# Kernel optimization log

Measured on AMD Instinct MI355X. Metric: run time of the kernel, lower is better.

The kernel has to match this reference:

```python
import jax, jax.numpy as jnp
import numpy as np

B, N, D, E, H, F, L = 4096, 32, 128, 256, 8, 1024, 6
DH = E // H  # head dim = 32
LN_EPS = 1e-5


def setup_inputs() -> dict:
    key = jax.random.key(0)
    ks = jax.random.split(key, 8)
    def s(k, shape, fan_in):
        return (jax.random.normal(k, shape, jnp.float32) / np.float32(np.sqrt(fan_in)))
    inp = {
        "obs": jax.random.normal(ks[0], (B, D), jnp.float32),
        "emb_W": s(ks[1], (N, D, E), D),          # per-node tokenizer Linear weights
        "emb_b": jnp.zeros((N, E), jnp.float32),
        "pos_emb": jax.random.normal(ks[2], (N, E), jnp.float32) * 0.02,
        "Wqkv": s(ks[3], (3 * E, E), E),          # shared across all L layers (torch code shares one layer object)
        "bqkv": jnp.zeros((3 * E,), jnp.float32),
        "Wo": s(ks[4], (E, E), E),
        "bo": jnp.zeros((E,), jnp.float32),
        "ln1_g": jnp.ones((E,), jnp.float32),
        "ln1_b": jnp.zeros((E,), jnp.float32),
        "ln2_g": jnp.ones((E,), jnp.float32),
        "ln2_b": jnp.zeros((E,), jnp.float32),
        "W1": s(ks[5], (E, F), E),
        "b1": jnp.zeros((F,), jnp.float32),
        "W2": s(ks[6], (F, E), F),
        "b2": jnp.zeros((E,), jnp.float32),
    }
    # kinematic-chain adjacency (|i-j|<=1) incl. forced self-loops, additive mask
    idx = jnp.arange(N)
    adj = jnp.abs(idx[:, None] - idx[None, :]) <= 1
    inp["adj_mask"] = jnp.where(adj, 0.0, -1e9).astype(jnp.float32)  # [N, N]
    return inp


def _layer_norm(x, g, b):
    m = jnp.mean(x, axis=-1, keepdims=True)
    v = jnp.var(x, axis=-1, keepdims=True)
    return (x - m) * jax.lax.rsqrt(v + LN_EPS) * g + b


def _encoder_layer(x, adj_mask, Wqkv, bqkv, Wo, bo, ln1_g, ln1_b, ln2_g, ln2_b, W1, b1, W2, b2):
    # pre-LN self-attention block
    h = _layer_norm(x, ln1_g, ln1_b)                      # [B, N, E]
    qkv = h @ Wqkv.T + bqkv                               # [B, N, 3E]
    q, k, v = jnp.split(qkv, 3, axis=-1)
    q = q.reshape(B, N, H, DH).transpose(0, 2, 1, 3)      # [B, H, N, DH]
    k = k.reshape(B, N, H, DH).transpose(0, 2, 1, 3)
    v = v.reshape(B, N, H, DH).transpose(0, 2, 1, 3)
    scale = np.float32(1.0 / np.sqrt(DH))
    scores = jnp.einsum('bhqd,bhkd->bhqk', q, k) * scale + adj_mask  # [B, H, N, N]
    attn = jax.nn.softmax(scores, axis=-1)
    o = jnp.einsum('bhqk,bhkd->bhqd', attn, v)
    o = o.transpose(0, 2, 1, 3).reshape(B, N, E)
    x = x + (o @ Wo.T + bo)
    # pre-LN feed-forward block (ReLU)
    h2 = _layer_norm(x, ln2_g, ln2_b)
    x = x + (jax.nn.relu(h2 @ W1 + b1) @ W2 + b2)
    return x


def reference(obs, emb_W, emb_b, pos_emb, Wqkv, bqkv, Wo, bo,
              ln1_g, ln1_b, ln2_g, ln2_b, W1, b1, W2, b2, adj_mask):
    # per-node MLP tokenizer (every node sees full obs): [B,D] x [N,D,E] -> [B,N,E]
    x = jnp.einsum('bd,nde->bne', obs, emb_W) + emb_b + pos_emb
    # BoT-Hard: all L layers masked; torch ModuleList shares a single layer's params
    for _ in range(L):
        x = _encoder_layer(x, adj_mask, Wqkv, bqkv, Wo, bo,
                           ln1_g, ln1_b, ln2_g, ln2_b, W1, b1, W2, b2)
    return x
```

## Files before the change

kernel.cpp:

```cpp
#include <hip/hip_runtime.h>
#include <hip/hip_bf16.h>
#include <stdint.h>

#define B_ 4096
#define N_ 32
#define D_ 128
#define E_ 256
#define H_ 8
#define F_ 1024
#define L_ 6
#define M_ (B_ * N_)

typedef unsigned short u16;
typedef __attribute__((ext_vector_type(8))) short short8;
typedef __attribute__((ext_vector_type(4))) short short4v;
typedef __attribute__((ext_vector_type(4))) float floatx4;

__device__ __forceinline__ float b2f(u16 u) {
  union { unsigned int i; float f; } c;
  c.i = ((unsigned int)u) << 16;
  return c.f;
}
__device__ __forceinline__ u16 f2b(float f) {
  union { float f; unsigned int i; } c;
  c.f = f;
  unsigned int x = c.i;
  return (u16)((x + 0x7fffu + ((x >> 16) & 1u)) >> 16);
}

template <bool RELU, bool RESID, bool OUTF32>
__global__ __launch_bounds__(256) void gemm_bt(
    const u16* __restrict__ A, int lda, long sAz,
    const u16* __restrict__ Bt, long sBz,
    const float* __restrict__ bias, long sBiasz,
    void* __restrict__ Cv, int ldc, long sCz,
    const float* __restrict__ resid,
    int K) {
  __shared__ u16 As[128 * 32];
  __shared__ u16 Bs[128 * 32];
  const int tid = threadIdx.x;
  const int wave = tid >> 6;
  const int lane = tid & 63;
  const int wm = wave & 1;
  const int wn = wave >> 1;
  const int lrow = lane & 15;
  const int quad = lane >> 4;
  const int z = blockIdx.z;
  const long m0 = (long)blockIdx.x * 128;
  const long n0 = (long)blockIdx.y * 128;

  const u16* Ab = A + (long)z * sAz + m0 * lda;
  const u16* Bb = Bt + (long)z * sBz + n0 * K;

  floatx4 acc[4][4];
#pragma unroll
  for (int a = 0; a < 4; ++a)
#pragma unroll
    for (int b = 0; b < 4; ++b) acc[a][b] = floatx4{0.f, 0.f, 0.f, 0.f};

  const int c0 = tid, c1 = tid + 256;
  const int r0 = c0 >> 2, o0 = (c0 & 3) * 8;
  const int r1 = c1 >> 2, o1 = (c1 & 3) * 8;

  for (int kb = 0; kb < K; kb += 32) {
    __syncthreads();
    short8 a0 = *(const short8*)(Ab + (long)r0 * lda + kb + o0);
    short8 a1 = *(const short8*)(Ab + (long)r1 * lda + kb + o1);
    short8 b0 = *(const short8*)(Bb + (long)r0 * K + kb + o0);
    short8 b1 = *(const short8*)(Bb + (long)r1 * K + kb + o1);
    *(short8*)(As + c0 * 8) = a0;
    *(short8*)(As + c1 * 8) = a1;
    *(short8*)(Bs + c0 * 8) = b0;
    *(short8*)(Bs + c1 * 8) = b1;
    __syncthreads();
    short8 af[4], bfr[4];
#pragma unroll
    for (int t = 0; t < 4; ++t) {
      af[t] = *(const short8*)(As + (wm * 64 + t * 16 + lrow) * 32 + quad * 8);
      bfr[t] = *(const short8*)(Bs + (wn * 64 + t * 16 + lrow) * 32 + quad * 8);
    }
#pragma unroll
    for (int tm = 0; tm < 4; ++tm)
#pragma unroll
      for (int tn = 0; tn < 4; ++tn)
        acc[tm][tn] = __builtin_amdgcn_mfma_f32_16x16x32_bf16(af[tm], bfr[tn], acc[tm][tn], 0, 0, 0);
  }

  const long cz = (long)z * sCz;
#pragma unroll
  for (int tn = 0; tn < 4; ++tn) {
    const long col = n0 + wn * 64 + tn * 16 + lrow;
    const float bv = bias[(long)z * sBiasz + col];
#pragma unroll
    for (int tm = 0; tm < 4; ++tm) {
#pragma unroll
      for (int r = 0; r < 4; ++r) {
        const long row = m0 + wm * 64 + tm * 16 + quad * 4 + r;
        float v = acc[tm][tn][r] + bv;
        if (RELU) v = fmaxf(v, 0.0f);
        const long idx = cz + row * (long)ldc + col;
        if (RESID) v += resid[idx];
        if (OUTF32)
          ((float*)Cv)[idx] = v;
        else
          ((u16*)Cv)[idx] = f2b(v);
      }
    }
  }
}

__global__ __launch_bounds__(256) void ln_kernel(const float* __restrict__ x,
                                                 const float* __restrict__ g,
                                                 const float* __restrict__ be,
                                                 u16* __restrict__ out) {
  const long row = ((long)blockIdx.x << 2) | (threadIdx.x >> 6);
  const int lane = threadIdx.x & 63;
  const float* xr = x + row * 256 + lane * 4;
  floatx4 v = *(const floatx4*)xr;
  float s = v[0] + v[1] + v[2] + v[3];
#pragma unroll
  for (int mk = 32; mk >= 1; mk >>= 1) s += __shfl_xor(s, mk, 64);
  const float mean = s * (1.0f / 256.0f);
  floatx4 d;
#pragma unroll
  for (int k = 0; k < 4; ++k) d[k] = v[k] - mean;
  float qs = d[0] * d[0] + d[1] * d[1] + d[2] * d[2] + d[3] * d[3];
#pragma unroll
  for (int mk = 32; mk >= 1; mk >>= 1) qs += __shfl_xor(qs, mk, 64);
  const float rstd = rsqrtf(qs * (1.0f / 256.0f) + 1e-5f);
  const int cb = lane * 4;
  const floatx4 gv = *(const floatx4*)(g + cb);
  const floatx4 bv = *(const floatx4*)(be + cb);
  short4v ov;
#pragma unroll
  for (int k = 0; k < 4; ++k)
    ov[k] = (short)f2b(d[k] * rstd * gv[k] + bv[k]);
  *(short4v*)(out + row * 256 + cb) = ov;
}

__global__ __launch_bounds__(256) void attn_kernel(const u16* __restrict__ qkv,
                                                   u16* __restrict__ o) {
  const int t = blockIdx.x * 256 + threadIdx.x;
  const int i = t & 31;
  const int h = (t >> 5) & 7;
  const long b = (long)(t >> 8);
  const long m = b * 32 + i;
  const u16* qp = qkv + m * 768 + h * 32;
  float q[32];
#pragma unroll
  for (int c = 0; c < 4; ++c) {
    short8 qv = *(const short8*)(qp + c * 8);
#pragma unroll
    for (int k = 0; k < 8; ++k) q[c * 8 + k] = b2f((u16)qv[k]);
  }
  float sc[3];
  int jc[3];
#pragma unroll
  for (int jj = 0; jj < 3; ++jj) {
    const int j = i - 1 + jj;
    const bool valid = (j >= 0) && (j < 32);
    const int jcl = valid ? j : i;
    jc[jj] = jcl;
    const u16* kp = qkv + (b * 32 + jcl) * 768 + 256 + h * 32;
    float dot = 0.0f;
#pragma unroll
    for (int c = 0; c < 4; ++c) {
      short8 kv = *(const short8*)(kp + c * 8);
#pragma unroll
      for (int k = 0; k < 8; ++k) dot += q[c * 8 + k] * b2f((u16)kv[k]);
    }
    sc[jj] = valid ? dot * 0.17677669529663687f : -3.0e38f;
  }
  const float mx = fmaxf(sc[0], fmaxf(sc[1], sc[2]));
  const float w0 = __expf(sc[0] - mx);
  const float w1 = __expf(sc[1] - mx);
  const float w2 = __expf(sc[2] - mx);
  const float inv = 1.0f / (w0 + w1 + w2);
  const float w[3] = {w0 * inv, w1 * inv, w2 * inv};
  float acc[32];
#pragma unroll
  for (int k = 0; k < 32; ++k) acc[k] = 0.0f;
#pragma unroll
  for (int jj = 0; jj < 3; ++jj) {
    const u16* vp = qkv + (b * 32 + jc[jj]) * 768 + 512 + h * 32;
    const float wj = w[jj];
#pragma unroll
    for (int c = 0; c < 4; ++c) {
      short8 vv = *(const short8*)(vp + c * 8);
#pragma unroll
      for (int k = 0; k < 8; ++k) acc[c * 8 + k] += wj * b2f((u16)vv[k]);
    }
  }
  u16* op = o + m * 256 + h * 32;
#pragma unroll
  for (int c = 0; c < 4; ++c) {
    short8 ov;
#pragma unroll
    for (int k = 0; k < 8; ++k) ov[k] = (short)f2b(acc[c * 8 + k]);
    *(short8*)(op + c * 8) = ov;
  }
}

__global__ __launch_bounds__(256) void transpose_f2b(const float* __restrict__ src,
                                                     u16* __restrict__ dst,
                                                     int R, int C) {
  const long base = (long)blockIdx.z * R * C;
  const int idx = blockIdx.x * 256 + threadIdx.x;
  if (idx < R * C) {
    const int r = idx / C;
    const int c = idx - r * C;
    dst[base + (long)c * R + r] = f2b(src[base + idx]);
  }
}

__global__ __launch_bounds__(256) void cvt_f2b_kernel(const float* __restrict__ s,
                                                      u16* __restrict__ d, int n) {
  const int i = blockIdx.x * 256 + threadIdx.x;
  if (i < n) d[i] = f2b(s[i]);
}

__global__ __launch_bounds__(256) void addf_kernel(const float* __restrict__ a,
                                                   const float* __restrict__ b,
                                                   float* __restrict__ d, int n) {
  const int i = blockIdx.x * 256 + threadIdx.x;
  if (i < n) d[i] = a[i] + b[i];
}

extern "C" void kernel_launch(void* const* d_in, const int* in_sizes, int n_in,
                              void* d_out, int out_size, void* d_ws, size_t ws_size,
                              hipStream_t stream) {
  (void)in_sizes; (void)n_in; (void)out_size; (void)ws_size;
  const float* obs   = (const float*)d_in[0];
  const float* emb_W = (const float*)d_in[1];
  const float* emb_b = (const float*)d_in[2];
  const float* pos   = (const float*)d_in[3];
  const float* Wqkv  = (const float*)d_in[4];
  const float* bqkv  = (const float*)d_in[5];
  const float* Wo    = (const float*)d_in[6];
  const float* bo    = (const float*)d_in[7];
  const float* ln1_g = (const float*)d_in[8];
  const float* ln1_b = (const float*)d_in[9];
  const float* ln2_g = (const float*)d_in[10];
  const float* ln2_b = (const float*)d_in[11];
  const float* W1    = (const float*)d_in[12];
  const float* b1    = (const float*)d_in[13];
  const float* W2    = (const float*)d_in[14];
  const float* b2    = (const float*)d_in[15];

  float* x = (float*)d_out;

  char* ws = (char*)d_ws;
  u16* hbuf   = (u16*)ws;   ws += (size_t)M_ * E_ * 2;
  u16* sbuf   = (u16*)ws;   ws += (size_t)M_ * F_ * 2;
  u16* embWt  = (u16*)ws;   ws += (size_t)N_ * D_ * E_ * 2;
  u16* obs_bf = (u16*)ws;   ws += (size_t)B_ * D_ * 2;
  u16* wqkv_bf= (u16*)ws;   ws += (size_t)3 * E_ * E_ * 2;
  u16* wo_bf  = (u16*)ws;   ws += (size_t)E_ * E_ * 2;
  u16* w1t    = (u16*)ws;   ws += (size_t)E_ * F_ * 2;
  u16* w2t    = (u16*)ws;   ws += (size_t)E_ * F_ * 2;
  float* cbias= (float*)ws; ws += (size_t)N_ * E_ * 4;

  transpose_f2b<<<dim3((D_ * E_ + 255) / 256, 1, N_), 256, 0, stream>>>(emb_W, embWt, D_, E_);
  transpose_f2b<<<dim3((E_ * F_ + 255) / 256, 1, 1), 256, 0, stream>>>(W1, w1t, E_, F_);
  transpose_f2b<<<dim3((E_ * F_ + 255) / 256, 1, 1), 256, 0, stream>>>(W2, w2t, F_, E_);
  cvt_f2b_kernel<<<(B_ * D_ + 255) / 256, 256, 0, stream>>>(obs, obs_bf, B_ * D_);
  cvt_f2b_kernel<<<(3 * E_ * E_ + 255) / 256, 256, 0, stream>>>(Wqkv, wqkv_bf, 3 * E_ * E_);
  cvt_f2b_kernel<<<(E_ * E_ + 255) / 256, 256, 0, stream>>>(Wo, wo_bf, E_ * E_);
  addf_kernel<<<(N_ * E_ + 255) / 256, 256, 0, stream>>>(emb_b, pos, cbias, N_ * E_);

  gemm_bt<false, false, true><<<dim3(B_ / 128, E_ / 128, N_), 256, 0, stream>>>(
      obs_bf, D_, 0, embWt, (long)E_ * D_, cbias, E_, x, N_ * E_, E_, nullptr, D_);

  for (int l = 0; l < L_; ++l) {
    ln_kernel<<<M_ / 4, 256, 0, stream>>>(x, ln1_g, ln1_b, hbuf);
    gemm_bt<false, false, false><<<dim3(M_ / 128, 768 / 128, 1), 256, 0, stream>>>(
        hbuf, E_, 0, wqkv_bf, 0, bqkv, 0, sbuf, 768, 0, nullptr, E_);
    attn_kernel<<<(M_ * H_) / 256, 256, 0, stream>>>(sbuf, hbuf);
    gemm_bt<false, true, true><<<dim3(M_ / 128, E_ / 128, 1), 256, 0, stream>>>(
        hbuf, E_, 0, wo_bf, 0, bo, 0, x, E_, 0, x, E_);
    ln_kernel<<<M_ / 4, 256, 0, stream>>>(x, ln2_g, ln2_b, hbuf);
    gemm_bt<true, false, false><<<dim3(M_ / 128, F_ / 128, 1), 256, 0, stream>>>(
        hbuf, E_, 0, w1t, 0, b1, 0, sbuf, F_, 0, nullptr, E_);
    gemm_bt<false, true, true><<<dim3(M_ / 128, E_ / 128, 1), 256, 0, stream>>>(
        sbuf, F_, 0, w2t, 0, b2, 0, x, E_, 0, x, F_);
  }
}
```

Baseline: 4.473 ms.

## Fuse LayerNorm into residual GEMM epilogues and stage tiles via global_load_lds

The standalone LayerNorm kernels are removed. The tokenizer, Wo and W2 GEMMs now use 512-thread blocks that each own a full 256-wide output row tile, reduce row sum and sum of squares through shared memory, and write both the fp32 residual stream and the bf16 normalized activations for the next GEMM. Tile staging in all GEMMs switches from register round-trips to direct global-to-LDS async loads. This saves a full fp32 read/write pass per LayerNorm, but variance now comes from E[x^2]-mean^2 and relies on correct async-load wait handling.

```diff
diff --git a/kernel.cpp b/kernel.cpp
--- a/kernel.cpp
+++ b/kernel.cpp
@@ -28,13 +28,18 @@
   return (u16)((x + 0x7fffu + ((x >> 16) & 1u)) >> 16);
 }
 
-template <bool RELU, bool RESID, bool OUTF32>
-__global__ __launch_bounds__(256) void gemm_bt(
-    const u16* __restrict__ A, int lda, long sAz,
-    const u16* __restrict__ Bt, long sBz,
-    const float* __restrict__ bias, long sBiasz,
-    void* __restrict__ Cv, int ldc, long sCz,
-    const float* __restrict__ resid,
+typedef __attribute__((address_space(1))) void* gas_ptr;
+typedef __attribute__((address_space(3))) void* las_ptr;
+__device__ __forceinline__ void async16(const u16* g, u16* l) {
+  __builtin_amdgcn_global_load_lds((gas_ptr)g, (las_ptr)l, 16, 0, 0);
+}
+
+template <bool RELU>
+__global__ __launch_bounds__(256) void gemm_async(
+    const u16* __restrict__ A, int lda,
+    const u16* __restrict__ Bt,
+    const float* __restrict__ bias,
+    u16* __restrict__ C, int ldc,
     int K) {
   __shared__ u16 As[128 * 32];
   __shared__ u16 Bs[128 * 32];
@@ -45,12 +50,11 @@
   const int wn = wave >> 1;
   const int lrow = lane & 15;
   const int quad = lane >> 4;
-  const int z = blockIdx.z;
   const long m0 = (long)blockIdx.x * 128;
   const long n0 = (long)blockIdx.y * 128;
 
-  const u16* Ab = A + (long)z * sAz + m0 * lda;
-  const u16* Bb = Bt + (long)z * sBz + n0 * K;
+  const u16* Ab = A + m0 * lda;
+  const u16* Bb = Bt + n0 * K;
 
   floatx4 acc[4][4];
 #pragma unroll
@@ -58,20 +62,19 @@
 #pragma unroll
     for (int b = 0; b < 4; ++b) acc[a][b] = floatx4{0.f, 0.f, 0.f, 0.f};
 
-  const int c0 = tid, c1 = tid + 256;
-  const int r0 = c0 >> 2, o0 = (c0 & 3) * 8;
-  const int r1 = c1 >> 2, o1 = (c1 & 3) * 8;
+  const int rr = tid >> 2;
+  const int oo = (tid & 3) * 8;
+  u16* lA0 = As + wave * 512;
+  u16* lA1 = As + 2048 + wave * 512;
+  u16* lB0 = Bs + wave * 512;
+  u16* lB1 = Bs + 2048 + wave * 512;
 
   for (int kb = 0; kb < K; kb += 32) {
     __syncthreads();
-    short8 a0 = *(const short8*)(Ab + (long)r0 * lda + kb + o0);
-    short8 a1 = *(const short8*)(Ab + (long)r1 * lda + kb + o1);
-    short8 b0 = *(const short8*)(Bb + (long)r0 * K + kb + o0);
-    short8 b1 = *(const short8*)(Bb + (long)r1 * K + kb + o1);
-    *(short8*)(As + c0 * 8) = a0;
-    *(short8*)(As + c1 * 8) = a1;
-    *(short8*)(Bs + c0 * 8) = b0;
-    *(short8*)(Bs + c1 * 8) = b1;
+    async16(Ab + (long)rr * lda + kb + oo, lA0);
+    async16(Ab + (long)(rr + 64) * lda + kb + oo, lA1);
+    async16(Bb + (long)rr * K + kb + oo, lB0);
+    async16(Bb + (long)(rr + 64) * K + kb + oo, lB1);
     __syncthreads();
     short8 af[4], bfr[4];
 #pragma unroll
@@ -86,11 +89,10 @@
         acc[tm][tn] = __builtin_amdgcn_mfma_f32_16x16x32_bf16(af[tm], bfr[tn], acc[tm][tn], 0, 0, 0);
   }
 
-  const long cz = (long)z * sCz;
 #pragma unroll
   for (int tn = 0; tn < 4; ++tn) {
     const long col = n0 + wn * 64 + tn * 16 + lrow;
-    const float bv = bias[(long)z * sBiasz + col];
+    const float bv = bias[col];
 #pragma unroll
     for (int tm = 0; tm < 4; ++tm) {
 #pragma unroll
@@ -98,44 +100,140 @@
         const long row = m0 + wm * 64 + tm * 16 + quad * 4 + r;
         float v = acc[tm][tn][r] + bv;
         if (RELU) v = fmaxf(v, 0.0f);
+        C[row * (long)ldc + col] = f2b(v);
+      }
+    }
+  }
+}
+
+template <bool RESID>
+__global__ __launch_bounds__(512) void gemm_ln(
+    const u16* __restrict__ A, int lda, long sAz,
+    const u16* __restrict__ Bt, long sBz,
+    const float* __restrict__ bias, long sBiasz,
+    float* __restrict__ xout, u16* __restrict__ hout,
+    int ldc, long sCz,
+    const float* __restrict__ resid,
+    const float* __restrict__ g, const float* __restrict__ be,
+    int K) {
+  __shared__ u16 As[128 * 32];
+  __shared__ u16 Bs[256 * 32];
+  __shared__ float part[128][4][2];
+  const int tid = threadIdx.x;
+  const int wave = tid >> 6;
+  const int lane = tid & 63;
+  const int wm = wave >> 2;
+  const int wn = wave & 3;
+  const int lrow = lane & 15;
+  const int quad = lane >> 4;
+  const int z = blockIdx.z;
+  const long m0 = (long)blockIdx.x * 128;
+
+  const u16* Ab = A + (long)z * sAz + m0 * lda;
+  const u16* Bb = Bt + (long)z * sBz;
+
+  floatx4 acc[4][4];
+#pragma unroll
+  for (int a = 0; a < 4; ++a)
+#pragma unroll
+    for (int b = 0; b < 4; ++b) acc[a][b] = floatx4{0.f, 0.f, 0.f, 0.f};
+
+  const int rr = tid >> 2;
+  const int oo = (tid & 3) * 8;
+  u16* lA = As + wave * 512;
+  u16* lB0 = Bs + wave * 512;
+  u16* lB1 = Bs + 4096 + wave * 512;
+
+  for (int kb = 0; kb < K; kb += 32) {
+    __syncthreads();
+    async16(Ab + (long)rr * lda + kb + oo, lA);
+    async16(Bb + (long)rr * K + kb + oo, lB0);
+    async16(Bb + (long)(rr + 128) * K + kb + oo, lB1);
+    __syncthreads();
+    short8 af[4], bfr[4];
+#pragma unroll
+    for (int t = 0; t < 4; ++t) {
+      af[t] = *(const short8*)(As + (wm * 64 + t * 16 + lrow) * 32 + quad * 8);
+      bfr[t] = *(const short8*)(Bs + (wn * 64 + t * 16 + lrow) * 32 + quad * 8);
+    }
+#pragma unroll
+    for (int tm = 0; tm < 4; ++tm)
+#pragma unroll
+      for (int tn = 0; tn < 4; ++tn)
+        acc[tm][tn] = __builtin_amdgcn_mfma_f32_16x16x32_bf16(af[tm], bfr[tn], acc[tm][tn], 0, 0, 0);
+  }
+
+  const long cz = (long)z * sCz;
+  float bv[4];
+#pragma unroll
+  for (int tn = 0; tn < 4; ++tn)
+    bv[tn] = bias[(long)z * sBiasz + wn * 64 + tn * 16 + lrow];
+#pragma unroll
+  for (int tm = 0; tm < 4; ++tm) {
+#pragma unroll
+    for (int r = 0; r < 4; ++r) {
+      const long row = m0 + wm * 64 + tm * 16 + quad * 4 + r;
+#pragma unroll
+      for (int tn = 0; tn < 4; ++tn) {
+        float v = acc[tm][tn][r] + bv[tn];
+        if (RESID) {
+          const long col = wn * 64 + tn * 16 + lrow;
+          v += resid[cz + row * (long)ldc + col];
+        }
+        acc[tm][tn][r] = v;
+      }
+    }
+  }
+
+#pragma unroll
+  for (int tm = 0; tm < 4; ++tm) {
+#pragma unroll
+    for (int r = 0; r < 4; ++r) {
+      float s = acc[tm][0][r] + acc[tm][1][r] + acc[tm][2][r] + acc[tm][3][r];
+      float q = acc[tm][0][r] * acc[tm][0][r] + acc[tm][1][r] * acc[tm][1][r] +
+                acc[tm][2][r] * acc[tm][2][r] + acc[tm][3][r] * acc[tm][3][r];
+#pragma unroll
+      for (int mk = 1; mk <= 8; mk <<= 1) {
+        s += __shfl_xor(s, mk, 64);
+        q += __shfl_xor(q, mk, 64);
+      }
+      if (lrow == 0) {
+        const int lr = wm * 64 + tm * 16 + quad * 4 + r;
+        part[lr][wn][0] = s;
+        part[lr][wn][1] = q;
+      }
+    }
+  }
+  __syncthreads();
+
+  float gv[4], bev[4];
+#pragma unroll
+  for (int tn = 0; tn < 4; ++tn) {
+    const int col = wn * 64 + tn * 16 + lrow;
+    gv[tn] = g[col];
+    bev[tn] = be[col];
+  }
+#pragma unroll
+  for (int tm = 0; tm < 4; ++tm) {
+#pragma unroll
+    for (int r = 0; r < 4; ++r) {
+      const int lr = wm * 64 + tm * 16 + quad * 4 + r;
+      const float s = part[lr][0][0] + part[lr][1][0] + part[lr][2][0] + part[lr][3][0];
+      const float q = part[lr][0][1] + part[lr][1][1] + part[lr][2][1] + part[lr][3][1];
+      const float mean = s * (1.0f / 256.0f);
+      const float var = q * (1.0f / 256.0f) - mean * mean;
+      const float rstd = rsqrtf(var + 1e-5f);
+      const long row = m0 + lr;
+#pragma unroll
+      for (int tn = 0; tn < 4; ++tn) {
+        const int col = wn * 64 + tn * 16 + lrow;
         const long idx = cz + row * (long)ldc + col;
-        if (RESID) v += resid[idx];
-        if (OUTF32)
-          ((float*)Cv)[idx] = v;
-        else
-          ((u16*)Cv)[idx] = f2b(v);
-      }
-    }
-  }
-}
-
-__global__ __launch_bounds__(256) void ln_kernel(const float* __restrict__ x,
-                                                 const float* __restrict__ g,
-                                                 const float* __restrict__ be,
-                                                 u16* __restrict__ out) {
-  const long row = ((long)blockIdx.x << 2) | (threadIdx.x >> 6);
-  const int lane = threadIdx.x & 63;
-  const float* xr = x + row * 256 + lane * 4;
-  floatx4 v = *(const floatx4*)xr;
-  float s = v[0] + v[1] + v[2] + v[3];
-#pragma unroll
-  for (int mk = 32; mk >= 1; mk >>= 1) s += __shfl_xor(s, mk, 64);
-  const float mean = s * (1.0f / 256.0f);
-  floatx4 d;
-#pragma unroll
-  for (int k = 0; k < 4; ++k) d[k] = v[k] - mean;
-  float qs = d[0] * d[0] + d[1] * d[1] + d[2] * d[2] + d[3] * d[3];
-#pragma unroll
-  for (int mk = 32; mk >= 1; mk >>= 1) qs += __shfl_xor(qs, mk, 64);
-  const float rstd = rsqrtf(qs * (1.0f / 256.0f) + 1e-5f);
-  const int cb = lane * 4;
-  const floatx4 gv = *(const floatx4*)(g + cb);
-  const floatx4 bv = *(const floatx4*)(be + cb);
-  short4v ov;
-#pragma unroll
-  for (int k = 0; k < 4; ++k)
-    ov[k] = (short)f2b(d[k] * rstd * gv[k] + bv[k]);
-  *(short4v*)(out + row * 256 + cb) = ov;
+        const float v = acc[tm][tn][r];
+        xout[idx] = v;
+        hout[idx] = f2b((v - mean) * rstd * gv[tn] + bev[tn]);
+      }
+    }
+  }
 }
 
 __global__ __launch_bounds__(256) void attn_kernel(const u16* __restrict__ qkv,
@@ -268,20 +366,21 @@
   cvt_f2b_kernel<<<(E_ * E_ + 255) / 256, 256, 0, stream>>>(Wo, wo_bf, E_ * E_);
   addf_kernel<<<(N_ * E_ + 255) / 256, 256, 0, stream>>>(emb_b, pos, cbias, N_ * E_);
 
-  gemm_bt<false, false, true><<<dim3(B_ / 128, E_ / 128, N_), 256, 0, stream>>>(
-      obs_bf, D_, 0, embWt, (long)E_ * D_, cbias, E_, x, N_ * E_, E_, nullptr, D_);
+  gemm_ln<false><<<dim3(B_ / 128, 1, N_), 512, 0, stream>>>(
+      obs_bf, D_, 0, embWt, (long)E_ * D_, cbias, E_,
+      x, hbuf, N_ * E_, E_, nullptr, ln1_g, ln1_b, D_);
 
   for (int l = 0; l < L_; ++l) {
-    ln_kernel<<<M_ / 4, 256, 0, stream>>>(x, ln1_g, ln1_b, hbuf);
-    gemm_bt<false, false, false><<<dim3(M_ / 128, 768 / 128, 1), 256, 0, stream>>>(
-        hbuf, E_, 0, wqkv_bf, 0, bqkv, 0, sbuf, 768, 0, nullptr, E_);
+    gemm_async<false><<<dim3(M_ / 128, 768 / 128, 1), 256, 0, stream>>>(
+        hbuf, E_, wqkv_bf, bqkv, sbuf, 768, E_);
     attn_kernel<<<(M_ * H_) / 256, 256, 0, stream>>>(sbuf, hbuf);
-    gemm_bt<false, true, true><<<dim3(M_ / 128, E_ / 128, 1), 256, 0, stream>>>(
-        hbuf, E_, 0, wo_bf, 0, bo, 0, x, E_, 0, x, E_);
-    ln_kernel<<<M_ / 4, 256, 0, stream>>>(x, ln2_g, ln2_b, hbuf);
-    gemm_bt<true, false, false><<<dim3(M_ / 128, F_ / 128, 1), 256, 0, stream>>>(
-        hbuf, E_, 0, w1t, 0, b1, 0, sbuf, F_, 0, nullptr, E_);
-    gemm_bt<false, true, true><<<dim3(M_ / 128, E_ / 128, 1), 256, 0, stream>>>(
-        sbuf, F_, 0, w2t, 0, b2, 0, x, E_, 0, x, F_);
-  }
-}
+    gemm_ln<true><<<dim3(M_ / 128, 1, 1), 512, 0, stream>>>(
+        hbuf, E_, 0, wo_bf, 0, bo, 0,
+        x, hbuf, E_, 0, x, ln2_g, ln2_b, E_);
+    gemm_async<true><<<dim3(M_ / 128, F_ / 128, 1), 256, 0, stream>>>(
+        hbuf, E_, w1t, b1, sbuf, F_, E_);
+    gemm_ln<true><<<dim3(M_ / 128, 1, 1), 512, 0, stream>>>(
+        sbuf, F_, 0, w2t, 0, b2, 0,
+        x, hbuf, E_, 0, x, ln1_g, ln1_b, F_);
+  }
+}
```

After: 4.266 ms. 4.6% less time.
